# Kernel optimization log

Measured on AMD Instinct MI355X. Metric: run time of the kernel, lower is better.

## Reference

```python
import jax, jax.numpy as jnp
import numpy as np

N = 20000   # atoms
E = 320000  # edges
G = 500     # molecules
D = 256     # node embedding depth
M = 128     # message depth
H = 4       # attention heads
DH = M // H
NR = 32     # radial basis functions
L = 4       # graph convolutions
T = 100     # atom types
EMB = 32    # atom type embedding dim
OUT = 512   # bottleneck dim
CUT = 6.0   # convolution cutoff (Angstrom)


def seg_softmax(logits, seg, num):
    m = jax.ops.segment_max(logits, seg, num_segments=num)
    e = jnp.exp(logits - m[seg])
    s = jax.ops.segment_sum(e, seg, num_segments=num)
    return e / (s[seg] + 1e-12)


def layernorm(x, eps=1e-5):
    mu = x.mean(-1, keepdims=True)
    var = ((x - mu) ** 2).mean(-1, keepdims=True)
    return (x - mu) * jax.lax.rsqrt(var + eps)


def setup_inputs() -> dict:
    key = jax.random.key(0)
    ks = jax.random.split(key, 20)
    s = 0.05
    pos = jax.random.normal(ks[0], (N, 3), dtype=jnp.float32) * 3.0
    z = jax.random.randint(ks[1], (N,), 0, T, dtype=jnp.int32)
    batch = jnp.sort(jax.random.randint(ks[2], (N,), 0, G, dtype=jnp.int32))
    edge_index = jax.random.randint(ks[3], (2, E), 0, N, dtype=jnp.int32)
    return {
        'pos': pos, 'z': z, 'batch': batch, 'edge_index': edge_index,
        'emb_table': jax.random.normal(ks[4], (T, EMB)) * s,
        'W_in': jax.random.normal(ks[5], (EMB + 3, D)) * s,
        'b_in': jnp.zeros((D,)),
        'Wq': jax.random.normal(ks[6], (L, D, M)) * s,
        'Wk': jax.random.normal(ks[7], (L, D, M)) * s,
        'Wv': jax.random.normal(ks[8], (L, D, M)) * s,
        'W_rbf': jax.random.normal(ks[9], (L, NR, M)) * s,
        'W_msg': jax.random.normal(ks[10], (L, M, D)) * s,
        'W_vgate': jax.random.normal(ks[11], (L, M, D)) * s,
        'W_vs': jax.random.normal(ks[12], (L, D, D)) * s,
        'W_node': jax.random.normal(ks[13], (L, D, D)) * s,
        'b_node': jnp.zeros((L, D)),
        'gamma': jnp.ones((L, D)),
        'w_att': jax.random.normal(ks[14], (D,)) * s,
        'W_out': jax.random.normal(ks[15], (D, OUT)) * s,
        'b_out': jnp.zeros((OUT,)),
    }


def reference(pos, z, batch, edge_index, emb_table, W_in, b_in, Wq, Wk, Wv,
              W_rbf, W_msg, W_vgate, W_vs, W_node, b_node, gamma, w_att,
              W_out, b_out):
    n = pos.shape[0]
    src, dst = edge_index[0], edge_index[1]
    # node init: atom-type embedding concat position -> linear
    h = jnp.concatenate([emb_table[z], pos], axis=-1) @ W_in + b_in  # [N,D]
    vfeat = jnp.zeros((n, 3, D), dtype=h.dtype)  # equivariant vector track
    # edge geometry + Bessel radial basis with cosine cutoff envelope
    rvec = pos[src] - pos[dst]                      # [E,3]
    dist = jnp.sqrt((rvec ** 2).sum(-1) + 1e-12)    # [E]
    unit = rvec / dist[:, None]
    freqs = jnp.arange(1, NR + 1, dtype=h.dtype) * (jnp.pi / CUT)
    env = jnp.where(dist < CUT, 0.5 * (jnp.cos(jnp.pi * dist / CUT) + 1.0), 0.0)
    rbf = jnp.sin(dist[:, None] * freqs) / dist[:, None] * env[:, None]  # [E,NR]
    inv_sqrt_dh = 1.0 / jnp.sqrt(jnp.asarray(DH, h.dtype))
    for l in range(L):
        ew = rbf @ W_rbf[l]                                   # [E,M] radial filter
        q = (h @ Wq[l])[dst].reshape(-1, H, DH)               # [E,H,DH]
        k = (h @ Wk[l])[src].reshape(-1, H, DH)
        vv = ((h @ Wv[l])[src] * ew).reshape(-1, H, DH)       # rbf-gated values
        logit = (q * k).sum(-1) * inv_sqrt_dh                 # [E,H]
        att = seg_softmax(logit, dst, n)                      # neighbor softmax per dest node
        me = (att[..., None] * vv).reshape(-1, M)             # [E,M] edge messages
        msg = jax.ops.segment_sum(me, dst, num_segments=n)    # [N,M]
        gate = me @ W_vgate[l]                                # [E,D]
        vfeat = vfeat + jax.ops.segment_sum(unit[:, :, None] * gate[:, None, :], dst, num_segments=n)
        upd = jax.nn.gelu(msg @ W_msg[l])                     # message -> node width
        upd = jax.nn.gelu(upd @ W_node[l] + b_node[l])        # nodewise FC layer
        vnorm = jnp.sqrt((vfeat ** 2).sum(1) + 1e-8)          # invariant vector norms [N,D]
        h = layernorm(h + upd + vnorm @ W_vs[l]) * gamma[l]
    # softmax graph aggregator -> bottleneck
    a = seg_softmax(h @ w_att, batch, G)                      # [N]
    pooled = jax.ops.segment_sum(a[:, None] * h, batch, num_segments=G)  # [G,D]
    return pooled @ W_out + b_out                             # [G,OUT]
```

## Files before the change

### kernel.cpp

```cpp
#include <hip/hip_runtime.h>
#include <math.h>

typedef unsigned char  u8;
typedef unsigned short u16;
typedef unsigned int   u32;
typedef __attribute__((ext_vector_type(8))) unsigned short ushort8;
typedef __attribute__((ext_vector_type(4))) unsigned short ushort4v;
typedef __attribute__((ext_vector_type(8))) short short8v;
typedef __attribute__((ext_vector_type(4))) float f32x4;
typedef __attribute__((ext_vector_type(2))) float f32x2;

__device__ __forceinline__ float gelu_f(float x) {
    const float c = 0.7978845608028654f;
    float x3 = x * x * x;
    float t = tanhf(c * (x + 0.044715f * x3));
    return 0.5f * x * (1.0f + t);
}

__device__ __forceinline__ u16 f2b(float f) {
    u32 u = __float_as_uint(f);
    return (u16)((u + 0x7FFFu + ((u >> 16) & 1u)) >> 16);
}
__device__ __forceinline__ float b2f(u16 u) {
    return __uint_as_float(((u32)u) << 16);
}

__device__ __forceinline__ u32 f2fp8_sw(float f) {
    u32 u = __float_as_uint(f);
    u32 s = (u >> 31) << 7;
    float af = fabsf(f);
    if (af >= 448.0f) return s | 0x7E;
    if (af < 0.015625f) {
        int m = __float2int_rn(af * 512.0f);
        if (m >= 8) return s | 0x08;
        return s | (u32)m;
    }
    u32 a = __float_as_uint(af);
    u32 r = a + 0xFFFFFu + ((a >> 20) & 1u);
    int e8 = (int)(r >> 23) - 120;
    u32 m3 = (r >> 20) & 7u;
    if (e8 >= 16) return s | 0x7E;
    return s | ((u32)e8 << 3) | m3;
}
__device__ __forceinline__ float fp8d_sw(u32 b) {
    u32 lo = b & 0x7Fu;
    u32 nb = (lo << 20) + 0x3C000000u;
    float n = __uint_as_float(nb | ((b & 0x80u) << 24));
    float sub = (float)(b & 7u) * 0.001953125f;
    sub = (b & 0x80u) ? -sub : sub;
    return (lo & 0x78u) ? n : sub;
}
__device__ __forceinline__ u8 f2fp8(float v) {
#if __has_builtin(__builtin_amdgcn_cvt_pk_fp8_f32)
    return (u8)(__builtin_amdgcn_cvt_pk_fp8_f32(v, v, 0, false) & 0xFF);
#else
    return (u8)f2fp8_sw(v);
#endif
}
__device__ __forceinline__ f32x2 kvdec(u32 pair) {
#if __has_builtin(__builtin_amdgcn_cvt_pk_f32_fp8)
    return __builtin_amdgcn_cvt_pk_f32_fp8((int)pair, false);
#else
    f32x2 r;
    r[0] = fp8d_sw(pair & 0xFF);
    r[1] = fp8d_sw((pair >> 8) & 0xFF);
    return r;
#endif
}

__device__ __forceinline__ void split_bf16(float f, u16& h, u16& l) {
    u32 u = __float_as_uint(f);
    u32 r = (u + 0x7FFFu + ((u >> 16) & 1u)) >> 16;
    h = (u16)r;
    float hf = __uint_as_float(r << 16);
    float d = f - hf;
    u32 u2 = __float_as_uint(d);
    l = (u16)((u2 + 0x7FFFu + ((u2 >> 16) & 1u)) >> 16);
}

__device__ __forceinline__ int xcd_swz(int orig, int nwg) {
    int q8 = nwg >> 3, r8 = nwg & 7;
    int xcd = orig & 7, ii = orig >> 3;
    return (xcd < r8 ? xcd * (q8 + 1) : r8 * (q8 + 1) + (xcd - r8) * q8) + ii;
}

__global__ __launch_bounds__(256) void zero_i32(int* __restrict__ p, int n) {
    int i = blockIdx.x * 256 + threadIdx.x;
    if (i < n) p[i] = 0;
}

struct TEntry { const float* src; u16* dh; u16* dl; int K; int N; };
struct TDesc  { TEntry e[29]; };

__global__ __launch_bounds__(256) void transpose_split(TDesc desc) {
    __shared__ float tile[32][33];
    TEntry en = desc.e[blockIdx.y];
    int tk = en.K >> 5, tn = en.N >> 5;
    int bx = blockIdx.x;
    if (bx >= tk * tn) return;
    int k0 = (bx % tk) * 32, n0 = (bx / tk) * 32;
    int tx = threadIdx.x & 31, ty = threadIdx.x >> 5;
    #pragma unroll
    for (int yy = 0; yy < 32; yy += 8)
        tile[ty + yy][tx] = en.src[(size_t)(k0 + ty + yy) * en.N + (n0 + tx)];
    __syncthreads();
    #pragma unroll
    for (int yy = 0; yy < 32; yy += 8) {
        int n = n0 + ty + yy, k = k0 + tx;
        float f = tile[tx][ty + yy];
        u16 h, l;
        split_bf16(f, h, l);
        en.dh[(size_t)n * en.K + k] = h;
        en.dl[(size_t)n * en.K + k] = l;
    }
}

__global__ __launch_bounds__(128) void build_rbf_table(
    const float* __restrict__ W_rbf, float* __restrict__ table)
{
    int k = blockIdx.x, l = blockIdx.y, m = threadIdx.x;
    const float* Wrbf_l = W_rbf + (size_t)l * 32 * 128;
    float* tbl = table + (size_t)l * 4098 * 128;
    const float PI = 3.14159265358979323846f;
    float d = fmaxf((float)k * (6.0f / 4096.0f), 1e-9f);
    float th = d * (PI / 6.0f);
    float s1, c1;
    __sincosf(th, &s1, &c1);
    float env = (d < 6.0f) ? (0.5f * c1 + 0.5f) : 0.0f;
    float invd = 1.0f / d;
    float two_c = 2.0f * c1;
    float sp = 0.f, sc = s1, dot = 0.f;
    #pragma unroll
    for (int r = 0; r < 32; ++r) {
        dot = fmaf(sc, Wrbf_l[r * 128 + m], dot);
        float sn = fmaf(two_c, sc, -sp);
        sp = sc; sc = sn;
    }
    tbl[(size_t)k * 128 + m] = dot * invd * env;
}

template<int OMODE, bool ACCUM, bool BIAS, bool DOGELU, bool SPLITB>
__global__ __launch_bounds__(256) void mfma_gemm(
    const u16* __restrict__ A, const u16* __restrict__ BH,
    const u16* __restrict__ BL, const float* __restrict__ bias,
    void* __restrict__ Cv, void* __restrict__ Cv2,
    int Mrows, int K, int Nc, int gx)
{
    __shared__ __align__(16) u16 sA [128][40];
    __shared__ __align__(16) u16 sBh[128][40];
    __shared__ __align__(16) u16 sBl[SPLITB ? 128 : 1][SPLITB ? 40 : 1];

    const int wg = xcd_swz(blockIdx.x, gridDim.x);
    const int r0 = (wg / gx) * 128, c0 = (wg % gx) * 128;

    const int t = threadIdx.x;
    const int lane = t & 63, wid = t >> 6;
    const int wr = (wid >> 1) * 64, wc = (wid & 1) * 64;

    f32x4 acc[4][4] = {};

    const int srow = t >> 1;
    const int skc  = (t & 1) * 16;

    for (int k0 = 0; k0 < K; k0 += 32) {
        {
            int gr = r0 + srow;
            ushort8 h0, h1;
            if (gr < Mrows) {
                const u16* p = A + (size_t)gr * K + (k0 + skc);
                h0 = *(const ushort8*)p;
                h1 = *(const ushort8*)(p + 8);
            } else {
                #pragma unroll
                for (int j = 0; j < 8; ++j) { h0[j] = 0; h1[j] = 0; }
            }
            *(ushort8*)&sA[srow][skc]     = h0;
            *(ushort8*)&sA[srow][skc + 8] = h1;
        }
        {
            int cg = c0 + srow;
            const u16* ph = BH + (size_t)cg * K + (k0 + skc);
            *(ushort8*)&sBh[srow][skc]     = *(const ushort8*)(ph);
            *(ushort8*)&sBh[srow][skc + 8] = *(const ushort8*)(ph + 8);
            if constexpr (SPLITB) {
                const u16* pl = BL + (size_t)cg * K + (k0 + skc);
                *(ushort8*)&sBl[srow][skc]     = *(const ushort8*)(pl);
                *(ushort8*)&sBl[srow][skc + 8] = *(const ushort8*)(pl + 8);
            }
        }
        __syncthreads();

        const int arow = wr + (lane & 15);
        const int koff = (lane >> 4) * 8;
        short8v ah[4];
        #pragma unroll
        for (int fr = 0; fr < 4; ++fr)
            ah[fr] = *(const short8v*)&sA[arow + fr * 16][koff];
        #pragma unroll
        for (int fc = 0; fc < 4; ++fc) {
            int bcol = wc + fc * 16 + (lane & 15);
            short8v bh = *(const short8v*)&sBh[bcol][koff];
            #pragma unroll
            for (int fr = 0; fr < 4; ++fr)
                acc[fr][fc] = __builtin_amdgcn_mfma_f32_16x16x32_bf16(ah[fr], bh, acc[fr][fc], 0, 0, 0);
            if constexpr (SPLITB) {
                short8v bl = *(const short8v*)&sBl[bcol][koff];
                #pragma unroll
                for (int fr = 0; fr < 4; ++fr)
                    acc[fr][fc] = __builtin_amdgcn_mfma_f32_16x16x32_bf16(ah[fr], bl, acc[fr][fc], 0, 0, 0);
            }
        }
        __syncthreads();
    }

    #pragma unroll
    for (int fr = 0; fr < 4; ++fr) {
        int rbase = r0 + wr + fr * 16 + (lane >> 4) * 4;
        #pragma unroll
        for (int fc = 0; fc < 4; ++fc) {
            int col = c0 + wc + fc * 16 + (lane & 15);
            #pragma unroll
            for (int reg = 0; reg < 4; ++reg) {
                int gr = rbase + reg;
                if (gr >= Mrows) continue;
                float v = acc[fr][fc][reg];
                if (BIAS)   v += bias[col];
                if (DOGELU) v = gelu_f(v);
                if (OMODE == 0) {
                    float* pc = (float*)Cv + (size_t)gr * Nc + col;
                    if (ACCUM) v += *pc;
                    *pc = v;
                } else if (OMODE == 1) {
                    ((u16*)Cv)[(size_t)gr * Nc + col] = f2b(v);
                } else if (OMODE == 2) {
                    u16* pc = (u16*)Cv + (size_t)gr * Nc + col;
                    *pc = f2b(v + b2f(*pc));
                } else {
                    if (col < 128)
                        ((u16*)Cv)[(size_t)gr * 128 + col] = f2b(v);
                    else if (col < 256)
                        ((u8*)Cv2)[(size_t)gr * 256 + (col - 128) * 2] = f2fp8(v);
                    else
                        ((u8*)Cv2)[(size_t)gr * 256 + (col - 256) * 2 + 1] = f2fp8(v);
                }
            }
        }
    }
}

__global__ __launch_bounds__(512) void vs_ln_kernel(
    const u16* __restrict__ A, const u16* __restrict__ BH,
    const u16* __restrict__ BL, const float* __restrict__ b2,
    const float* __restrict__ gamma_l, u16* __restrict__ h16, int Mrows)
{
    __shared__ __align__(16) u16 sA [128][40];
    __shared__ __align__(16) u16 sBh[256][40];
    __shared__ __align__(16) u16 sBl[256][40];
    __shared__ float sSum[128][4];
    __shared__ float sSq [128][4];

    const int r0 = blockIdx.x * 128;
    const int t = threadIdx.x;
    const int lane = t & 63, wid = t >> 6;
    const int wr = (wid >> 2) * 64, wc = (wid & 3) * 64;

    f32x4 acc[4][4] = {};
    const int K = 256;
    const int srow = t >> 2;
    const int skc  = (t & 3) * 8;

    for (int k0 = 0; k0 < K; k0 += 32) {
        {
            int gr = r0 + srow;
            ushort8 h0;
            #pragma unroll
            for (int j = 0; j < 8; ++j) h0[j] = 0;
            if (gr < Mrows) h0 = *(const ushort8*)(A + (size_t)gr * K + k0 + skc);
            *(ushort8*)&sA[srow][skc] = h0;
        }
        {
            *(ushort8*)&sBh[srow][skc]       = *(const ushort8*)(BH + (size_t)srow * K + k0 + skc);
            *(ushort8*)&sBh[srow + 128][skc] = *(const ushort8*)(BH + (size_t)(srow + 128) * K + k0 + skc);
            *(ushort8*)&sBl[srow][skc]       = *(const ushort8*)(BL + (size_t)srow * K + k0 + skc);
            *(ushort8*)&sBl[srow + 128][skc] = *(const ushort8*)(BL + (size_t)(srow + 128) * K + k0 + skc);
        }
        __syncthreads();

        const int arow = wr + (lane & 15);
        const int koff = (lane >> 4) * 8;
        short8v ah[4];
        #pragma unroll
        for (int fr = 0; fr < 4; ++fr)
            ah[fr] = *(const short8v*)&sA[arow + fr * 16][koff];
        #pragma unroll
        for (int fc = 0; fc < 4; ++fc) {
            int bcol = wc + fc * 16 + (lane & 15);
            short8v bh = *(const short8v*)&sBh[bcol][koff];
            short8v bl = *(const short8v*)&sBl[bcol][koff];
            #pragma unroll
            for (int fr = 0; fr < 4; ++fr) {
                acc[fr][fc] = __builtin_amdgcn_mfma_f32_16x16x32_bf16(ah[fr], bh, acc[fr][fc], 0, 0, 0);
                acc[fr][fc] = __builtin_amdgcn_mfma_f32_16x16x32_bf16(ah[fr], bl, acc[fr][fc], 0, 0, 0);
            }
        }
        __syncthreads();
    }

    float psum[4][4] = {}, psq[4][4] = {};
    #pragma unroll
    for (int fr = 0; fr < 4; ++fr) {
        #pragma unroll
        for (int fc = 0; fc < 4; ++fc) {
            int col = wc + fc * 16 + (lane & 15);
            #pragma unroll
            for (int reg = 0; reg < 4; ++reg) {
                int gr = r0 + wr + fr * 16 + (lane >> 4) * 4 + reg;
                float x = 0.f;
                if (gr < Mrows) {
                    size_t ix = (size_t)gr * 256 + col;
                    x = acc[fr][fc][reg] + b2[ix] + b2f(h16[ix]);
                }
                acc[fr][fc][reg] = x;
                psum[fr][reg] += x;
                psq[fr][reg]  = fmaf(x, x, psq[fr][reg]);
            }
        }
    }
    #pragma unroll
    for (int fr = 0; fr < 4; ++fr) {
        #pragma unroll
        for (int reg = 0; reg < 4; ++reg) {
            float s = psum[fr][reg], sq = psq[fr][reg];
            #pragma unroll
            for (int off = 8; off; off >>= 1) {
                s  += __shfl_xor(s, off);
                sq += __shfl_xor(sq, off);
            }
            psum[fr][reg] = s; psq[fr][reg] = sq;
        }
    }
    if ((lane & 15) == 0) {
        int qg = lane >> 4;
        #pragma unroll
        for (int fr = 0; fr < 4; ++fr) {
            #pragma unroll
            for (int reg = 0; reg < 4; ++reg) {
                int row = wr + fr * 16 + qg * 4 + reg;
                sSum[row][wc >> 6] = psum[fr][reg];
                sSq [row][wc >> 6] = psq[fr][reg];
            }
        }
    }
    __syncthreads();
    #pragma unroll
    for (int fr = 0; fr < 4; ++fr) {
        #pragma unroll
        for (int reg = 0; reg < 4; ++reg) {
            int row = wr + fr * 16 + (lane >> 4) * 4 + reg;
            int gr = r0 + row;
            if (gr >= Mrows) continue;
            float S = sSum[row][0] + sSum[row][1] + sSum[row][2] + sSum[row][3];
            float Q = sSq[row][0] + sSq[row][1] + sSq[row][2] + sSq[row][3];
            float mu = S * (1.0f / 256.0f);
            float var = fmaxf(Q * (1.0f / 256.0f) - mu * mu, 0.0f);
            float rs = rsqrtf(var + 1e-5f);
            #pragma unroll
            for (int fc = 0; fc < 4; ++fc) {
                int col = wc + fc * 16 + (lane & 15);
                float y = (acc[fr][fc][reg] - mu) * rs * gamma_l[col];
                h16[(size_t)gr * 256 + col] = f2b(y);
            }
        }
    }
}

__global__ void hist_edges(const int* __restrict__ ei, int* __restrict__ deg, int E_) {
    int e = blockIdx.x * 256 + threadIdx.x;
    if (e < E_) atomicAdd(&deg[ei[E_ + e]], 1);
}
__global__ void hist_nodes(const int* __restrict__ batch, int* __restrict__ gcnt, int n) {
    int i = blockIdx.x * 256 + threadIdx.x;
    if (i < n) atomicAdd(&gcnt[batch[i]], 1);
}

__global__ __launch_bounds__(1024) void scan_kernel(
    const int* __restrict__ cnt, int n, int* __restrict__ out, int* __restrict__ cursor)
{
    __shared__ int part[1024];
    int t = threadIdx.x;
    int chunk = (n + 1023) / 1024;
    int base = t * chunk;
    int s = 0;
    for (int k = 0; k < chunk; ++k) { int i = base + k; if (i < n) s += cnt[i]; }
    part[t] = s;
    __syncthreads();
    for (int off = 1; off < 1024; off <<= 1) {
        int u = (t >= off) ? part[t - off] : 0;
        __syncthreads();
        part[t] += u;
        __syncthreads();
    }
    int run = part[t] - s;
    for (int k = 0; k < chunk; ++k) {
        int i = base + k;
        if (i < n) {
            out[i] = run;
            if (cursor) cursor[i] = run;
            run += cnt[i];
        }
    }
    if (t == 1023) out[n] = part[1023];
}

__global__ void scatter_kernel(const int* __restrict__ ei, int* __restrict__ cursor,
                               int2* __restrict__ perm2, int E_) {
    int e = blockIdx.x * 256 + threadIdx.x;
    if (e < E_) {
        int p = atomicAdd(&cursor[ei[E_ + e]], 1);
        perm2[p] = make_int2(e, ei[e]);
    }
}

__global__ __launch_bounds__(256) void geom_kernel(
    const float* __restrict__ pos, const int* __restrict__ ei,
    float4* __restrict__ eg, int E_)
{
    int e = blockIdx.x * 256 + threadIdx.x;
    if (e >= E_) return;
    int s = ei[e], dn = ei[E_ + e];
    float dx = pos[s * 3 + 0] - pos[dn * 3 + 0];
    float dy = pos[s * 3 + 1] - pos[dn * 3 + 1];
    float dz = pos[s * 3 + 2] - pos[dn * 3 + 2];
    float d = sqrtf(dx * dx + dy * dy + dz * dz + 1e-12f);
    float invd = 1.0f / d;
    eg[e] = make_float4(dx * invd, dy * invd, dz * invd, d);
}

__global__ __launch_bounds__(256) void init_h_kernel(
    const int* __restrict__ z, const float* __restrict__ pos,
    const float* __restrict__ emb, const float* __restrict__ W_in,
    const float* __restrict__ b_in, u16* __restrict__ h16)
{
    int i = blockIdx.x, d = threadIdx.x;
    float acc = b_in[d];
    int zi = z[i];
    #pragma unroll 8
    for (int k = 0; k < 32; ++k)
        acc += emb[zi * 32 + k] * W_in[k * 256 + d];
    #pragma unroll
    for (int x = 0; x < 3; ++x)
        acc += pos[i * 3 + x] * W_in[(32 + x) * 256 + d];
    h16[(size_t)i * 256 + d] = f2b(acc);
}

__global__ __launch_bounds__(128) void edge_attn_kernel(
    const int* __restrict__ rowptr, const int2* __restrict__ perm2,
    const u16* __restrict__ q16, const u16* __restrict__ kv8,
    const float4* __restrict__ eg, const float* __restrict__ table_l,
    u16* __restrict__ msg, u16* __restrict__ U)
{
    int m = threadIdx.x;
    int i = blockIdx.x;

    int p0 = rowptr[i], p1 = rowptr[i + 1];
    float q = b2f(q16[(size_t)i * 128 + m]);
    float Mx = -1e30f, S = 0.f, am = 0.f, a0 = 0.f, a1 = 0.f, a2 = 0.f;
    const float iscale = 0.1767766952966369f;

    for (int p = p0; p < p1; p += 8) {
        int rem = p1 - p;
        int ee[8], jj[8];
        #pragma unroll
        for (int u = 0; u < 8; ++u) {
            int pp = p + (u < rem ? u : 0);
            int2 pe = perm2[pp];
            ee[u] = __builtin_amdgcn_readfirstlane(pe.x);
            jj[u] = __builtin_amdgcn_readfirstlane(pe.y);
        }
        u32 kv[8];
        float4 g[8];
        #pragma unroll
        for (int u = 0; u < 8; ++u) {
            kv[u] = kv8[(size_t)jj[u] * 128 + m];
            g[u]  = eg[ee[u]];
        }
        float lg[8], vd[8];
        #pragma unroll
        for (int u = 0; u < 8; ++u) {
            f32x2 c = kvdec(kv[u]);
            vd[u] = c[1];
            float pr = q * c[0];
            #pragma unroll
            for (int off = 16; off; off >>= 1) pr += __shfl_xor(pr, off);
            lg[u] = pr * iscale;
        }
        float ew[8];
        #pragma unroll
        for (int u = 0; u < 8; ++u) {
            float x = fminf(g[u].w * (4096.0f / 6.0f), 4096.0f);
            int b = (int)x;
            float tf = x - (float)b;
            float f0 = table_l[(size_t)b * 128 + m];
            float f1 = table_l[(size_t)(b + 1) * 128 + m];
            ew[u] = fmaf(tf, f1 - f0, f0);
        }
        float Mb = Mx;
        #pragma unroll
        for (int u = 0; u < 8; ++u) Mb = fmaxf(Mb, lg[u]);
        float sc = __expf(Mx - Mb);
        float w[8];
        #pragma unroll
        for (int u = 0; u < 8; ++u)
            w[u] = (u < rem) ? __expf(lg[u] - Mb) : 0.f;
        float ws = 0.f, wvs = 0.f, wx = 0.f, wy = 0.f, wz = 0.f;
        #pragma unroll
        for (int u = 0; u < 8; ++u) {
            float wv = w[u] * vd[u] * ew[u];
            ws  += w[u];
            wvs += wv;
            wx = fmaf(wv, g[u].x, wx);
            wy = fmaf(wv, g[u].y, wy);
            wz = fmaf(wv, g[u].z, wz);
        }
        S  = S  * sc + ws;
        am = am * sc + wvs;
        a0 = a0 * sc + wx;
        a1 = a1 * sc + wy;
        a2 = a2 * sc + wz;
        Mx = Mb;
    }
    float inv = 1.0f / (S + 1e-12f);
    msg[(size_t)i * 128 + m] = f2b(am * inv);
    U[((size_t)i * 3 + 0) * 128 + m] = f2b(a0 * inv);
    U[((size_t)i * 3 + 1) * 128 + m] = f2b(a1 * inv);
    U[((size_t)i * 3 + 2) * 128 + m] = f2b(a2 * inv);
}

__global__ __launch_bounds__(256) void vnorm_kernel(
    const u16* __restrict__ vf16, u16* __restrict__ vn)
{
    int i = blockIdx.x, d = threadIdx.x;
    float v0 = b2f(vf16[((size_t)i * 3 + 0) * 256 + d]);
    float v1 = b2f(vf16[((size_t)i * 3 + 1) * 256 + d]);
    float v2 = b2f(vf16[((size_t)i * 3 + 2) * 256 + d]);
    vn[(size_t)i * 256 + d] = f2b(sqrtf(v0 * v0 + v1 * v1 + v2 * v2 + 1e-8f));
}

__global__ __launch_bounds__(256) void pool_kernel(
    const u16* __restrict__ h16, const float* __restrict__ w_att,
    const int* __restrict__ gptr, u16* __restrict__ pooled)
{
    __shared__ float sM[4], sS[4];
    __shared__ float sAcc[4][256];
    int g = blockIdx.x;
    int t = threadIdx.x, w = t >> 6, lane = t & 63;
    int c0 = lane * 4;
    int n0 = gptr[g], n1 = gptr[g + 1];
    float4 wa = *(const float4*)(w_att + c0);
    float M = -1e30f, S = 0.f, a0 = 0.f, a1 = 0.f, a2 = 0.f, a3 = 0.f;
    for (int i = n0 + w; i < n1; i += 4) {
        ushort4v hv = *(const ushort4v*)(h16 + (size_t)i * 256 + c0);
        float h0 = b2f(hv[0]), h1 = b2f(hv[1]), h2 = b2f(hv[2]), h3 = b2f(hv[3]);
        float p = h0 * wa.x + h1 * wa.y + h2 * wa.z + h3 * wa.w;
        #pragma unroll
        for (int off = 32; off; off >>= 1) p += __shfl_xor(p, off);
        float nM = fmaxf(M, p);
        float sc = __expf(M - nM), wg = __expf(p - nM);
        S = S * sc + wg;
        a0 = a0 * sc + wg * h0;
        a1 = a1 * sc + wg * h1;
        a2 = a2 * sc + wg * h2;
        a3 = a3 * sc + wg * h3;
        M = nM;
    }
    sAcc[w][c0 + 0] = a0; sAcc[w][c0 + 1] = a1;
    sAcc[w][c0 + 2] = a2; sAcc[w][c0 + 3] = a3;
    if (lane == 0) { sM[w] = M; sS[w] = S; }
    __syncthreads();
    if (w == 0) {
        float Mg = fmaxf(fmaxf(sM[0], sM[1]), fmaxf(sM[2], sM[3]));
        float e0 = __expf(sM[0] - Mg), e1 = __expf(sM[1] - Mg);
        float e2 = __expf(sM[2] - Mg), e3 = __expf(sM[3] - Mg);
        float St = sS[0] * e0 + sS[1] * e1 + sS[2] * e2 + sS[3] * e3;
        float inv = 1.0f / (St + 1e-12f);
        #pragma unroll
        for (int c = 0; c < 4; ++c) {
            float v = sAcc[0][c0 + c] * e0 + sAcc[1][c0 + c] * e1
                    + sAcc[2][c0 + c] * e2 + sAcc[3][c0 + c] * e3;
            pooled[(size_t)g * 256 + c0 + c] = f2b(v * inv);
        }
    }
}

extern "C" void kernel_launch(void* const* d_in, const int* in_sizes, int n_in,
                              void* d_out, int out_size, void* d_ws, size_t ws_size,
                              hipStream_t stream)
{
    const float* pos   = (const float*)d_in[0];
    const int*   z     = (const int*)d_in[1];
    const int*   batch = (const int*)d_in[2];
    const int*   ei    = (const int*)d_in[3];
    const float* emb   = (const float*)d_in[4];
    const float* W_in  = (const float*)d_in[5];
    const float* b_in  = (const float*)d_in[6];
    const float* Wq    = (const float*)d_in[7];
    const float* Wk    = (const float*)d_in[8];
    const float* Wv    = (const float*)d_in[9];
    const float* W_rbf = (const float*)d_in[10];
    const float* W_msg = (const float*)d_in[11];
    const float* W_vg  = (const float*)d_in[12];
    const float* W_vs  = (const float*)d_in[13];
    const float* W_nd  = (const float*)d_in[14];
    const float* b_nd  = (const float*)d_in[15];
    const float* gam   = (const float*)d_in[16];
    const float* watt  = (const float*)d_in[17];
    const float* W_out = (const float*)d_in[18];
    const float* b_out = (const float*)d_in[19];

    const int N = in_sizes[0] / 3;
    const int E = in_sizes[3] / 2;
    const int G = out_size / 512;

    char* ws = (char*)d_ws;
    size_t o = 0;
    auto alloc = [&](size_t bytes) -> char* {
        o = (o + 255) & ~(size_t)255;
        char* r = ws + o;
        o += bytes;
        return r;
    };
    float4* f_eg   = (float4*)alloc((size_t)E * 16);
    u16*   h16     = (u16*)  alloc((size_t)N * 256 * 2);
    u16*   vf16    = (u16*)  alloc((size_t)N * 3 * 256 * 2);
    u16*   q16     = (u16*)  alloc((size_t)N * 128 * 2);
    u16*   kv8     = (u16*)  alloc((size_t)N * 128 * 2);
    u16*   umb     = (u16*)  alloc((size_t)N * 4 * 128 * 2);
    u16*   b1_16   = (u16*)  alloc((size_t)N * 256 * 2);
    float* f_b2    = (float*)alloc((size_t)N * 256 * 4);
    u16*   vn16    = (u16*)  alloc((size_t)N * 256 * 2);
    u16*   pool16  = (u16*)  alloc((size_t)G * 256 * 2);
    float* f_table = (float*)alloc((size_t)4 * 4098 * 128 * 4);
    const size_t LS = 384 * 256 + 2 * (256 * 128) + 2 * (256 * 256);
    const size_t OFF_QKV = 0, OFF_VG = 384 * 256, OFF_MSG = OFF_VG + 256 * 128,
                 OFF_ND = OFF_MSG + 256 * 128, OFF_VS = OFF_ND + 256 * 256;
    const size_t OFF_OUT = LS * 4;
    u16* whi = (u16*)alloc((LS * 4 + 512 * 256) * sizeof(u16));
    u16* wlo = (u16*)alloc((LS * 4 + 512 * 256) * sizeof(u16));
    int*  i_deg   = (int*)alloc((size_t)N * 4);
    int*  i_rowp  = (int*)alloc((size_t)(N + 1) * 4);
    int*  i_cur   = (int*)alloc((size_t)(N + 1) * 4);
    int2* i_perm2 = (int2*)alloc((size_t)E * 8);
    int*  i_gcnt  = (int*)alloc((size_t)G * 4);
    int*  i_gptr  = (int*)alloc((size_t)(G + 1) * 4);

    u16* U16   = umb;
    u16* msg16 = umb + (size_t)3 * N * 128;

    TDesc td;
    int idx = 0;
    for (int l = 0; l < 4; ++l) {
        u16* bh = whi + (size_t)l * LS;
        u16* bl = wlo + (size_t)l * LS;
        td.e[idx++] = { Wq   + (size_t)l * 256 * 128, bh + OFF_QKV,             bl + OFF_QKV,             256, 128 };
        td.e[idx++] = { Wk   + (size_t)l * 256 * 128, bh + OFF_QKV + 128 * 256, bl + OFF_QKV + 128 * 256, 256, 128 };
        td.e[idx++] = { Wv   + (size_t)l * 256 * 128, bh + OFF_QKV + 256 * 256, bl + OFF_QKV + 256 * 256, 256, 128 };
        td.e[idx++] = { W_vg + (size_t)l * 128 * 256, bh + OFF_VG,  bl + OFF_VG,  128, 256 };
        td.e[idx++] = { W_msg+ (size_t)l * 128 * 256, bh + OFF_MSG, bl + OFF_MSG, 128, 256 };
        td.e[idx++] = { W_nd + (size_t)l * 256 * 256, bh + OFF_ND,  bl + OFF_ND,  256, 256 };
        td.e[idx++] = { W_vs + (size_t)l * 256 * 256, bh + OFF_VS,  bl + OFF_VS,  256, 256 };
    }
    td.e[idx++] = { W_out, whi + OFF_OUT, wlo + OFF_OUT, 256, 512 };

    zero_i32<<<(N + 255) / 256, 256, 0, stream>>>(i_deg, N);
    zero_i32<<<(G + 255) / 256, 256, 0, stream>>>(i_gcnt, G);
    transpose_split<<<dim3(128, 29), 256, 0, stream>>>(td);
    build_rbf_table<<<dim3(4098, 4), 128, 0, stream>>>(W_rbf, f_table);

    hist_edges<<<(E + 255) / 256, 256, 0, stream>>>(ei, i_deg, E);
    scan_kernel<<<1, 1024, 0, stream>>>(i_deg, N, i_rowp, i_cur);
    scatter_kernel<<<(E + 255) / 256, 256, 0, stream>>>(ei, i_cur, i_perm2, E);
    hist_nodes<<<(N + 255) / 256, 256, 0, stream>>>(batch, i_gcnt, N);
    scan_kernel<<<1, 1024, 0, stream>>>(i_gcnt, G, i_gptr, (int*)nullptr);
    geom_kernel<<<(E + 255) / 256, 256, 0, stream>>>(pos, ei, f_eg, E);
    init_h_kernel<<<N, 256, 0, stream>>>(z, pos, emb, W_in, b_in, h16);

    const int MB  = (N + 127) / 128;
    const int MB3 = (3 * N + 127) / 128;
    const int MBG = (G + 127) / 128;

    for (int l = 0; l < 4; ++l) {
        u16* bh = whi + (size_t)l * LS;
        u16* bl = wlo + (size_t)l * LS;
        const float* bnd_l = b_nd + (size_t)l * 256;
        const float* gam_l = gam  + (size_t)l * 256;
        const float* tbl_l = f_table + (size_t)l * 4098 * 128;

        mfma_gemm<3,false,false,false,false><<<3 * MB, 256, 0, stream>>>(
            h16, bh + OFF_QKV, nullptr, nullptr, q16, kv8, N, 256, 384, 3);

        edge_attn_kernel<<<N, 128, 0, stream>>>(i_rowp, i_perm2, q16, kv8,
                                                f_eg, tbl_l, msg16, U16);

        if (l == 0)
            mfma_gemm<1,false,false,false,false><<<2 * MB3, 256, 0, stream>>>(
                U16, bh + OFF_VG, nullptr, nullptr, vf16, nullptr, 3 * N, 128, 256, 2);
        else
            mfma_gemm<2,false,false,false,false><<<2 * MB3, 256, 0, stream>>>(
                U16, bh + OFF_VG, nullptr, nullptr, vf16, nullptr, 3 * N, 128, 256, 2);

        mfma_gemm<1,false,false,true,false><<<2 * MB, 256, 0, stream>>>(
            msg16, bh + OFF_MSG, nullptr, nullptr, b1_16, nullptr, N, 128, 256, 2);
        mfma_gemm<0,false,true,true,true><<<2 * MB, 256, 0, stream>>>(
            b1_16, bh + OFF_ND, bl + OFF_ND, bnd_l, f_b2, nullptr, N, 256, 256, 2);
        vnorm_kernel<<<N, 256, 0, stream>>>(vf16, vn16);
        vs_ln_kernel<<<MB, 512, 0, stream>>>(
            vn16, bh + OFF_VS, bl + OFF_VS, f_b2, gam_l, h16, N);
    }

    pool_kernel<<<G, 256, 0, stream>>>(h16, watt, i_gptr, pool16);
    mfma_gemm<0,false,true,false,true><<<4 * MBG, 256, 0, stream>>>(
        pool16, whi + OFF_OUT, wlo + OFF_OUT, b_out, (float*)d_out, nullptr, G, 256, 512, 4);
}
```

Before: 955.7 us.

## Stage bf16 GEMM outputs through LDS for vector stores; store node FC output as bf16

For the bf16 output modes, the GEMM epilogue now writes the tile into shared memory, then writes it to global memory with 16-byte vector stores and vectorised read-modify-write in accumulate mode. The old path issued scattered 2-byte stores. The node FC output buffer changes from fp32 to bf16, which halves its write and read traffic in the vs/layernorm kernel at some precision cost. The two zeroing kernels are also merged into one launch. The staging adds a barrier and LDS reuse in the epilogue.

```diff
diff --git a/kernel.cpp b/kernel.cpp
--- a/kernel.cpp
+++ b/kernel.cpp
@@ -84,9 +84,11 @@
     return (xcd < r8 ? xcd * (q8 + 1) : r8 * (q8 + 1) + (xcd - r8) * q8) + ii;
 }
 
-__global__ __launch_bounds__(256) void zero_i32(int* __restrict__ p, int n) {
+__global__ __launch_bounds__(256) void zero2_i32(int* __restrict__ a, int na,
+                                                 int* __restrict__ b, int nb) {
     int i = blockIdx.x * 256 + threadIdx.x;
-    if (i < n) p[i] = 0;
+    if (i < na) a[i] = 0;
+    else if (i - na < nb) b[i - na] = 0;
 }
 
 struct TEntry { const float* src; u16* dh; u16* dl; int K; int N; };
@@ -146,9 +148,15 @@
     void* __restrict__ Cv, void* __restrict__ Cv2,
     int Mrows, int K, int Nc, int gx)
 {
-    __shared__ __align__(16) u16 sA [128][40];
-    __shared__ __align__(16) u16 sBh[128][40];
-    __shared__ __align__(16) u16 sBl[SPLITB ? 128 : 1][SPLITB ? 40 : 1];
+    constexpr bool STAGE_OUT = (OMODE == 1 || OMODE == 2);
+    constexpr int MAIN_B = 128 * 40 * 2 * (SPLITB ? 3 : 2);
+    constexpr int OUT_B  = STAGE_OUT ? 128 * 136 * 2 : 0;
+    constexpr int SMEM_B = (MAIN_B > OUT_B) ? MAIN_B : OUT_B;
+    __shared__ __align__(16) char smem[SMEM_B];
+    u16 (*sA)[40]  = (u16(*)[40])smem;
+    u16 (*sBh)[40] = (u16(*)[40])(smem + 128 * 40 * 2);
+    u16 (*sBl)[40] = (u16(*)[40])(smem + 2 * 128 * 40 * 2);
+    u16 (*sOut)[136] = (u16(*)[136])smem;
 
     const int wg = xcd_swz(blockIdx.x, gridDim.x);
     const int r0 = (wg / gx) * 128, c0 = (wg % gx) * 128;
@@ -213,35 +221,71 @@
         __syncthreads();
     }
 
-    #pragma unroll
-    for (int fr = 0; fr < 4; ++fr) {
-        int rbase = r0 + wr + fr * 16 + (lane >> 4) * 4;
-        #pragma unroll
-        for (int fc = 0; fc < 4; ++fc) {
-            int col = c0 + wc + fc * 16 + (lane & 15);
-            #pragma unroll
-            for (int reg = 0; reg < 4; ++reg) {
-                int gr = rbase + reg;
-                if (gr >= Mrows) continue;
-                float v = acc[fr][fc][reg];
-                if (BIAS)   v += bias[col];
-                if (DOGELU) v = gelu_f(v);
-                if (OMODE == 0) {
-                    float* pc = (float*)Cv + (size_t)gr * Nc + col;
-                    if (ACCUM) v += *pc;
-                    *pc = v;
-                } else if (OMODE == 1) {
-                    ((u16*)Cv)[(size_t)gr * Nc + col] = f2b(v);
-                } else if (OMODE == 2) {
-                    u16* pc = (u16*)Cv + (size_t)gr * Nc + col;
-                    *pc = f2b(v + b2f(*pc));
-                } else {
-                    if (col < 128)
-                        ((u16*)Cv)[(size_t)gr * 128 + col] = f2b(v);
-                    else if (col < 256)
-                        ((u8*)Cv2)[(size_t)gr * 256 + (col - 128) * 2] = f2fp8(v);
-                    else
-                        ((u8*)Cv2)[(size_t)gr * 256 + (col - 256) * 2 + 1] = f2fp8(v);
+    if constexpr (STAGE_OUT) {
+        #pragma unroll
+        for (int fr = 0; fr < 4; ++fr) {
+            int rbase = wr + fr * 16 + (lane >> 4) * 4;
+            #pragma unroll
+            for (int fc = 0; fc < 4; ++fc) {
+                int col = wc + fc * 16 + (lane & 15);
+                #pragma unroll
+                for (int reg = 0; reg < 4; ++reg) {
+                    float v = acc[fr][fc][reg];
+                    if (BIAS)   v += bias[c0 + col];
+                    if (DOGELU) v = gelu_f(v);
+                    sOut[rbase + reg][col] = f2b(v);
+                }
+            }
+        }
+        __syncthreads();
+        #pragma unroll
+        for (int p = 0; p < 4; ++p) {
+            int row = p * 32 + (t >> 3);
+            int cch = (t & 7) * 16;
+            int gr = r0 + row;
+            if (gr < Mrows) {
+                u16* gp = (u16*)Cv + (size_t)gr * Nc + c0 + cch;
+                ushort8 v0 = *(ushort8*)&sOut[row][cch];
+                ushort8 v1 = *(ushort8*)&sOut[row][cch + 8];
+                if (OMODE == 2) {
+                    ushort8 o0 = *(const ushort8*)gp;
+                    ushort8 o1 = *(const ushort8*)(gp + 8);
+                    #pragma unroll
+                    for (int j = 0; j < 8; ++j) {
+                        v0[j] = f2b(b2f(v0[j]) + b2f(o0[j]));
+                        v1[j] = f2b(b2f(v1[j]) + b2f(o1[j]));
+                    }
+                }
+                *(ushort8*)gp       = v0;
+                *(ushort8*)(gp + 8) = v1;
+            }
+        }
+    } else {
+        #pragma unroll
+        for (int fr = 0; fr < 4; ++fr) {
+            int rbase = r0 + wr + fr * 16 + (lane >> 4) * 4;
+            #pragma unroll
+            for (int fc = 0; fc < 4; ++fc) {
+                int col = c0 + wc + fc * 16 + (lane & 15);
+                #pragma unroll
+                for (int reg = 0; reg < 4; ++reg) {
+                    int gr = rbase + reg;
+                    if (gr >= Mrows) continue;
+                    float v = acc[fr][fc][reg];
+                    if (BIAS)   v += bias[col];
+                    if (DOGELU) v = gelu_f(v);
+                    if (OMODE == 0) {
+                        float* pc = (float*)Cv + (size_t)gr * Nc + col;
+                        if (ACCUM) v += *pc;
+                        *pc = v;
+                    } else {
+                        if (col < 128)
+                            ((u16*)Cv)[(size_t)gr * 128 + col] = f2b(v);
+                        else if (col < 256)
+                            ((u8*)Cv2)[(size_t)gr * 256 + (col - 128) * 2] = f2fp8(v);
+                        else
+                            ((u8*)Cv2)[(size_t)gr * 256 + (col - 256) * 2 + 1] = f2fp8(v);
+                    }
                 }
             }
         }
@@ -250,7 +294,7 @@
 
 __global__ __launch_bounds__(512) void vs_ln_kernel(
     const u16* __restrict__ A, const u16* __restrict__ BH,
-    const u16* __restrict__ BL, const float* __restrict__ b2,
+    const u16* __restrict__ BL, const u16* __restrict__ b2,
     const float* __restrict__ gamma_l, u16* __restrict__ h16, int Mrows)
 {
     __shared__ __align__(16) u16 sA [128][40];
@@ -318,7 +362,7 @@
                 float x = 0.f;
                 if (gr < Mrows) {
                     size_t ix = (size_t)gr * 256 + col;
-                    x = acc[fr][fc][reg] + b2[ix] + b2f(h16[ix]);
+                    x = acc[fr][fc][reg] + b2f(b2[ix]) + b2f(h16[ix]);
                 }
                 acc[fr][fc][reg] = x;
                 psum[fr][reg] += x;
@@ -636,7 +680,7 @@
     u16*   kv8     = (u16*)  alloc((size_t)N * 128 * 2);
     u16*   umb     = (u16*)  alloc((size_t)N * 4 * 128 * 2);
     u16*   b1_16   = (u16*)  alloc((size_t)N * 256 * 2);
-    float* f_b2    = (float*)alloc((size_t)N * 256 * 4);
+    u16*   b2_16   = (u16*)  alloc((size_t)N * 256 * 2);
     u16*   vn16    = (u16*)  alloc((size_t)N * 256 * 2);
     u16*   pool16  = (u16*)  alloc((size_t)G * 256 * 2);
     float* f_table = (float*)alloc((size_t)4 * 4098 * 128 * 4);
@@ -671,8 +715,7 @@
     }
     td.e[idx++] = { W_out, whi + OFF_OUT, wlo + OFF_OUT, 256, 512 };
 
-    zero_i32<<<(N + 255) / 256, 256, 0, stream>>>(i_deg, N);
-    zero_i32<<<(G + 255) / 256, 256, 0, stream>>>(i_gcnt, G);
+    zero2_i32<<<(N + G + 255) / 256, 256, 0, stream>>>(i_deg, N, i_gcnt, G);
     transpose_split<<<dim3(128, 29), 256, 0, stream>>>(td);
     build_rbf_table<<<dim3(4098, 4), 128, 0, stream>>>(W_rbf, f_table);
 
@@ -710,11 +753,11 @@
 
         mfma_gemm<1,false,false,true,false><<<2 * MB, 256, 0, stream>>>(
             msg16, bh + OFF_MSG, nullptr, nullptr, b1_16, nullptr, N, 128, 256, 2);
-        mfma_gemm<0,false,true,true,true><<<2 * MB, 256, 0, stream>>>(
-            b1_16, bh + OFF_ND, bl + OFF_ND, bnd_l, f_b2, nullptr, N, 256, 256, 2);
+        mfma_gemm<1,false,true,true,true><<<2 * MB, 256, 0, stream>>>(
+            b1_16, bh + OFF_ND, bl + OFF_ND, bnd_l, b2_16, nullptr, N, 256, 256, 2);
         vnorm_kernel<<<N, 256, 0, stream>>>(vf16, vn16);
         vs_ln_kernel<<<MB, 512, 0, stream>>>(
-            vn16, bh + OFF_VS, bl + OFF_VS, f_b2, gam_l, h16, N);
+            vn16, bh + OFF_VS, bl + OFF_VS, b2_16, gam_l, h16, N);
     }
 
     pool_kernel<<<G, 256, 0, stream>>>(h16, watt, i_gptr, pool16);
```

Result: faster. 834.6 us (-12.7%).
